# Kernel tuning notes

Hardware: AMD Instinct MI355X
Metric: run time of the kernel (lower is better)

## Reference

```python
import jax, jax.numpy as jnp
import numpy as np

N_NODES = 50000
N_EDGES = 800000
D_IN = 512
D_HID = 256


def gcn_conv(x, W, b, src, dst, n_nodes):
    """PyG-style GCNConv: self-loops + symmetric normalization.
    x: [N, d_in], W: [d_in, d_out], b: [d_out], src/dst: [E] (already include self-loops? no -> add here)
    """
    loops = jnp.arange(n_nodes, dtype=src.dtype)
    src_f = jnp.concatenate([src, loops])  # [E+N]
    dst_f = jnp.concatenate([dst, loops])
    deg = jax.ops.segment_sum(jnp.ones_like(dst_f, dtype=x.dtype), dst_f,
                              num_segments=n_nodes)  # [N]
    dinv = jnp.where(deg > 0, jax.lax.rsqrt(deg), 0.0)
    norm = dinv[src_f] * dinv[dst_f]  # [E+N]
    h = x @ W  # [N, d_out] -- dense GEMM
    msg = h[src_f] * norm[:, None]  # gather + scale, [E+N, d_out]
    out = jax.ops.segment_sum(msg, dst_f, num_segments=n_nodes)  # scatter-add
    return out + b


def setup_inputs() -> dict:
    key = jax.random.key(0)
    k1, k2, k3, k4, k5 = jax.random.split(key, 5)
    x = jax.random.normal(k1, (N_NODES, D_IN), dtype=jnp.float32)
    edge_index = jax.random.randint(k2, (2, N_EDGES), 0, N_NODES, dtype=jnp.int32)
    # Glorot-ish init for weights
    W1 = jax.random.normal(k3, (D_IN, D_HID), dtype=jnp.float32) / np.sqrt(D_IN)
    W2 = jax.random.normal(k4, (D_HID, D_HID), dtype=jnp.float32) / np.sqrt(D_HID)
    b1 = jnp.zeros((D_HID,), dtype=jnp.float32)
    b2 = jnp.zeros((D_HID,), dtype=jnp.float32)
    return {"x": x, "edge_index": edge_index, "W1": W1, "b1": b1, "W2": W2, "b2": b2}


def reference(x, edge_index, W1, b1, W2, b2):
    n_nodes = x.shape[0]
    src, dst = edge_index[0], edge_index[1]
    h = jax.nn.relu(gcn_conv(x, W1, b1, src, dst, n_nodes))
    h = gcn_conv(h, W2, b2, src, dst, n_nodes)
    # edge-level gather-dot scoring
    score = jnp.einsum('ed,ed->e', h[src], h[dst])  # [E]
    prob_edge = jax.nn.sigmoid(score)
    return prob_edge
```

## Files before the change

kernel.cpp:

```cpp
#include <hip/hip_runtime.h>
#include <stdint.h>

#define D_IN 512
#define D_HID 256

typedef __attribute__((ext_vector_type(8))) short bf16x8;
typedef __attribute__((ext_vector_type(8))) unsigned short u16x8;
typedef __attribute__((ext_vector_type(4))) float f32x4;

__device__ __forceinline__ float b2f(unsigned short u) {
    union { float f; uint32_t i; } x; x.i = ((uint32_t)u) << 16; return x.f;
}
__device__ __forceinline__ unsigned short f2b(float f) {
    union { float f; uint32_t i; } x; x.f = f;
    uint32_t i = x.i;
    uint32_t r = (i + 0x7FFFu + ((i >> 16) & 1u)) >> 16;
    return (unsigned short)r;
}

__device__ __forceinline__ void async_copy16(const unsigned short* g, unsigned short* lds) {
    __builtin_amdgcn_global_load_lds((const __attribute__((address_space(1))) unsigned int*)g,
                                     (__attribute__((address_space(3))) unsigned int*)lds,
                                     16, 0, 0);
}

__global__ __launch_bounds__(256) void detect_dtype_kernel(const ushort4* __restrict__ raw,
                                                           int n4, int* __restrict__ flag) {
    int i = blockIdx.x * blockDim.x + threadIdx.x;
    int hit = 0;
    if (i < n4) {
        ushort4 u = raw[i];
        hit = ((((u.x >> 7) & 0xFF) == 0xFF) || (((u.y >> 7) & 0xFF) == 0xFF) ||
               (((u.z >> 7) & 0xFF) == 0xFF) || (((u.w >> 7) & 0xFF) == 0xFF)) ? 1 : 0;
    }
    unsigned long long b = __ballot(hit);
    if ((threadIdx.x & 63) == 0 && b != 0ULL) atomicOr(flag, 1);
}

__global__ __launch_bounds__(256) void xcast_kernel(const void* __restrict__ X,
        unsigned short* __restrict__ xh, int n4, const int* __restrict__ flag) {
    int i = blockIdx.x * blockDim.x + threadIdx.x;
    if (i >= n4) return;
    ushort4 o;
    if (*flag != 0) {
        float4 v = ((const float4*)X)[i];
        o.x = f2b(v.x); o.y = f2b(v.y); o.z = f2b(v.z); o.w = f2b(v.w);
    } else {
        o = ((const ushort4*)X)[i];
    }
    ((ushort4*)xh)[i] = o;
}

__global__ void hist_kernel(const int* __restrict__ dst, int* __restrict__ counts, int E) {
    int e = blockIdx.x * blockDim.x + threadIdx.x;
    if (e < E) atomicAdd(&counts[dst[e]], 1);
}

__global__ __launch_bounds__(256) void partial_sum_kernel(const int* __restrict__ counts,
        int* __restrict__ partial, int n) {
    __shared__ int sh[4];
    int b = blockIdx.x;
    int lane = threadIdx.x & 63, wv = threadIdx.x >> 6;
    int s = 0;
    for (int j = threadIdx.x; j < 1024; j += 256) {
        int i = b * 1024 + j;
        s += (i < n) ? counts[i] : 0;
    }
#pragma unroll
    for (int off = 32; off > 0; off >>= 1) s += __shfl_down(s, off, 64);
    if (lane == 0) sh[wv] = s;
    __syncthreads();
    if (threadIdx.x == 0) partial[b] = sh[0] + sh[1] + sh[2] + sh[3];
}

__global__ void scan_partials_kernel(int* __restrict__ partial, int nb,
                                     int* __restrict__ indptr, int N) {
    int lane = threadIdx.x & 63;
    int orig = (lane < nb) ? partial[lane] : 0;
    int v = orig;
#pragma unroll
    for (int off = 1; off < 64; off <<= 1) {
        int u = __shfl(v, lane - off, 64);
        if (lane >= off) v += u;
    }
    int tot = __shfl(v, nb - 1, 64);
    if (lane < nb) partial[lane] = v - orig;
    if (lane == 0) indptr[N] = tot;
}

__global__ __launch_bounds__(1024) void scan_chunk_kernel(const int* __restrict__ counts,
        const int* __restrict__ partial, int* __restrict__ indptr, int* __restrict__ cursor,
        float* __restrict__ dinv, int n) {
    __shared__ int sh[1024];
    int b = blockIdx.x;
    int i = b * 1024 + threadIdx.x;
    int v = (i < n) ? counts[i] : 0;
    sh[threadIdx.x] = v;
    __syncthreads();
    for (int off = 1; off < 1024; off <<= 1) {
        int t = (threadIdx.x >= off) ? sh[threadIdx.x - off] : 0;
        __syncthreads();
        sh[threadIdx.x] += t;
        __syncthreads();
    }
    if (i < n) {
        int e = partial[b] + sh[threadIdx.x] - v;
        indptr[i] = e;
        cursor[i] = e;
        dinv[i] = rsqrtf((float)(v + 1));
    }
}

__global__ void scatter_kernel(const int* __restrict__ src, const int* __restrict__ dst,
                               int* __restrict__ cursor, int* __restrict__ csr_src,
                               int* __restrict__ csr_dst, int* __restrict__ csr_eid, int E) {
    int e = blockIdx.x * blockDim.x + threadIdx.x;
    if (e < E) {
        int d = dst[e];
        int pos = atomicAdd(&cursor[d], 1);
        csr_src[pos] = src[e];
        csr_dst[pos] = d;
        csr_eid[pos] = e;
    }
}

__global__ void wT_kernel(const void* __restrict__ W, unsigned short* __restrict__ WT,
                          int K, const int* __restrict__ flag) {
    int idx = blockIdx.x * blockDim.x + threadIdx.x;
    if (idx >= K * 256) return;
    int k = idx >> 8;
    int n = idx & 255;
    float v = (*flag != 0) ? ((const float*)W)[idx] : b2f(((const unsigned short*)W)[idx]);
    WT[n * K + k] = f2b(v);
}

template<int K>
__global__ __launch_bounds__(256) void gemm_bf16(const unsigned short* __restrict__ A,
        const unsigned short* __restrict__ WT, unsigned short* __restrict__ C, int M) {
    __shared__ unsigned short As[2][64 * 64];
    constexpr int NK = K / 64;
    int t = threadIdx.x;
    int lane = t & 63, wv = t >> 6;
    int n0 = lane & 15, grp = lane >> 4;
    int row0 = blockIdx.x * 64;

    int srow = wv * 16 + (lane >> 3);
    int segp = lane & 7;

    f32x4 acc[4][4];
#pragma unroll
    for (int rt = 0; rt < 4; ++rt)
#pragma unroll
        for (int ct = 0; ct < 4; ++ct) acc[rt][ct] = (f32x4){0.f, 0.f, 0.f, 0.f};

#pragma unroll
    for (int j = 0; j < 2; ++j) {
        int row = srow + j * 8;
        int s = (segp - row) & 7;
        const unsigned short* g = A + (size_t)min(row0 + row, M - 1) * K + s * 8;
        async_copy16(g, &As[0][0] + wv * 1024 + j * 512);
    }
    asm volatile("s_waitcnt vmcnt(0)" ::: "memory");
    __builtin_amdgcn_s_barrier();

    for (int kk = 0; kk < NK; ++kk) {
        int cur = kk & 1;
        if (kk + 1 < NK) {
            int kof = (kk + 1) * 64;
#pragma unroll
            for (int j = 0; j < 2; ++j) {
                int row = srow + j * 8;
                int s = (segp - row) & 7;
                const unsigned short* g = A + (size_t)min(row0 + row, M - 1) * K + kof + s * 8;
                async_copy16(g, &As[cur ^ 1][0] + wv * 1024 + j * 512);
            }
        }
        int kof = kk * 64;
        bf16x8 bw[4][2];
#pragma unroll
        for (int ct = 0; ct < 4; ++ct)
#pragma unroll
            for (int h = 0; h < 2; ++h)
                bw[ct][h] = *(const bf16x8*)(WT + (size_t)((wv * 4 + ct) * 16 + n0) * K
                                             + kof + h * 32 + grp * 8);
#pragma unroll
        for (int rt = 0; rt < 4; ++rt) {
            int r = rt * 16 + n0;
#pragma unroll
            for (int h = 0; h < 2; ++h) {
                int sp = (h * 4 + grp + r) & 7;
                bf16x8 a = *(const bf16x8*)(&As[cur][0] + r * 64 + sp * 8);
#pragma unroll
                for (int ct = 0; ct < 4; ++ct)
                    acc[rt][ct] = __builtin_amdgcn_mfma_f32_16x16x32_bf16(a, bw[ct][h],
                                                                          acc[rt][ct], 0, 0, 0);
            }
        }
        asm volatile("s_waitcnt vmcnt(0)" ::: "memory");
        __builtin_amdgcn_s_barrier();
    }
#pragma unroll
    for (int rt = 0; rt < 4; ++rt) {
#pragma unroll
        for (int ct = 0; ct < 4; ++ct) {
#pragma unroll
            for (int reg = 0; reg < 4; ++reg) {
                int row = row0 + rt * 16 + grp * 4 + reg;
                if (row < M)
                    C[(size_t)row * 256 + (wv * 4 + ct) * 16 + n0] = f2b(acc[rt][ct][reg]);
            }
        }
    }
}

__global__ __launch_bounds__(256) void aggregate_kernel(const unsigned short* __restrict__ h,
        const int* __restrict__ indptr, const int* __restrict__ csr_src,
        const float* __restrict__ dinv, const void* __restrict__ bias,
        unsigned short* __restrict__ out, int n, int do_relu, const int* __restrict__ flag) {
    int wave = threadIdx.x >> 6;
    int lane = threadIdx.x & 63;
    int half = lane >> 5;
    int hl = lane & 31;
    int v = blockIdx.x * 4 + wave;
    if (v >= n) return;
    int beg = indptr[v];
    int end = indptr[v + 1];
    float dv = dinv[v];

    float acc[8];
    if (half == 0) {
        u16x8 hv = *(const u16x8*)(h + (size_t)v * 256 + hl * 8);
#pragma unroll
        for (int i = 0; i < 8; ++i) acc[i] = dv * b2f(hv[i]);
    } else {
#pragma unroll
        for (int i = 0; i < 8; ++i) acc[i] = 0.f;
    }

    int eA = beg + half;
    float w0 = 0.f, w1 = 0.f, w2 = 0.f;
    u16x8 r0, r1, r2;
    if (eA < end) {
        int s = csr_src[eA];
        w0 = dinv[s];
        r0 = *(const u16x8*)(h + (size_t)s * 256 + hl * 8);
    }
    if (eA + 2 < end) {
        int s = csr_src[eA + 2];
        w1 = dinv[s];
        r1 = *(const u16x8*)(h + (size_t)s * 256 + hl * 8);
    }
    if (eA + 4 < end) {
        int s = csr_src[eA + 4];
        w2 = dinv[s];
        r2 = *(const u16x8*)(h + (size_t)s * 256 + hl * 8);
    }
    for (int e = eA; e < end; e += 2) {
#pragma unroll
        for (int i = 0; i < 8; ++i) acc[i] += w0 * b2f(r0[i]);
        w0 = w1; r0 = r1;
        w1 = w2; r1 = r2;
        int en = e + 6;
        if (en < end) {
            int s = csr_src[en];
            w2 = dinv[s];
            r2 = *(const u16x8*)(h + (size_t)s * 256 + hl * 8);
        }
    }

#pragma unroll
    for (int i = 0; i < 8; ++i) acc[i] += __shfl_xor(acc[i], 32, 64);

    if (half == 0) {
        float bb[8];
        if (*flag != 0) {
            const float* bp = (const float*)bias + hl * 8;
#pragma unroll
            for (int i = 0; i < 8; ++i) bb[i] = bp[i];
        } else {
            const unsigned short* bp = (const unsigned short*)bias + hl * 8;
#pragma unroll
            for (int i = 0; i < 8; ++i) bb[i] = b2f(bp[i]);
        }
        u16x8 ov;
#pragma unroll
        for (int i = 0; i < 8; ++i) {
            float o = dv * acc[i] + bb[i];
            if (do_relu) o = fmaxf(o, 0.f);
            ov[i] = f2b(o);
        }
        *(u16x8*)(out + (size_t)v * 256 + hl * 8) = ov;
    }
}

__global__ __launch_bounds__(256) void edge_score_mfma(const unsigned short* __restrict__ h,
        const int* __restrict__ csr_src, const int* __restrict__ csr_dst,
        const int* __restrict__ csr_eid,
        void* __restrict__ out, int E, const int* __restrict__ flag) {
    int lane = threadIdx.x & 63;
    int wv = threadIdx.x >> 6;
    int base = (blockIdx.x * 4 + wv) * 16;
    if (base >= E) return;
    int m = lane & 15, grp = lane >> 4;
    int e = base + m;
    int ec = min(e, E - 1);
    int s = csr_src[ec], d = csr_dst[ec];
    int eid = csr_eid[ec];
    const unsigned short* hs = h + (size_t)s * 256 + grp * 8;
    const unsigned short* hd = h + (size_t)d * 256 + grp * 8;
    f32x4 acc = {0.f, 0.f, 0.f, 0.f};
#pragma unroll
    for (int kk = 0; kk < 8; ++kk) {
        bf16x8 a = *(const bf16x8*)(hs + kk * 32);
        bf16x8 b = *(const bf16x8*)(hd + kk * 32);
        acc = __builtin_amdgcn_mfma_f32_16x16x32_bf16(a, b, acc, 0, 0, 0);
    }
    int reg = m - grp * 4;
    if (reg >= 0 && reg < 4 && e < E) {
        float p = (reg == 0) ? acc[0] : (reg == 1) ? acc[1] : (reg == 2) ? acc[2] : acc[3];
        float prob = 1.f / (1.f + __expf(-p));
        if (*flag != 0)
            ((float*)out)[eid] = prob;
        else
            ((unsigned short*)out)[eid] = f2b(prob);
    }
}

extern "C" void kernel_launch(void* const* d_in, const int* in_sizes, int n_in,
                              void* d_out, int out_size, void* d_ws, size_t ws_size,
                              hipStream_t stream) {
    const void* x  = d_in[0];
    const int* edge_index = (const int*)d_in[1];
    const void* W1 = d_in[2];
    const void* b1 = d_in[3];
    const void* W2 = d_in[4];
    const void* b2 = d_in[5];

    const int N = in_sizes[0] / D_IN;
    const int E = in_sizes[1] / 2;
    const int* src = edge_index;
    const int* dst = edge_index + E;

    char* ws = (char*)d_ws;
    size_t off = 0;
    auto alloc = [&](size_t bytes) {
        char* p = ws + off;
        off = (off + bytes + 255) & ~(size_t)255;
        return p;
    };
    int* flag     = (int*)alloc(256);
    float* dinv   = (float*)alloc((size_t)N * 4);
    int* counts   = (int*)alloc((size_t)N * 4);
    int* indptr   = (int*)alloc((size_t)(N + 1) * 4);
    int* cursor   = (int*)alloc((size_t)N * 4);
    int* partial  = (int*)alloc(64 * 4);
    int* csr_src  = (int*)alloc((size_t)E * 4);
    int* csr_dst  = (int*)alloc((size_t)E * 4);
    int* csr_eid  = (int*)alloc((size_t)E * 4);
    unsigned short* W1T = (unsigned short*)alloc((size_t)D_IN * 256 * 2);
    unsigned short* W2T = (unsigned short*)alloc((size_t)D_HID * 256 * 2);
    unsigned short* xh  = (unsigned short*)alloc((size_t)N * D_IN * 2);
    unsigned short* hA  = (unsigned short*)alloc((size_t)N * 256 * 2);
    unsigned short* hB  = (unsigned short*)alloc((size_t)N * 256 * 2);

    const int nb = (N + 1023) / 1024;

    hipMemsetAsync(flag, 0, 4, stream);
    hipMemsetAsync(counts, 0, (size_t)N * 4, stream);
    detect_dtype_kernel<<<64, 256, 0, stream>>>((const ushort4*)x, 16384, flag);
    xcast_kernel<<<(N * D_IN / 4 + 255) / 256, 256, 0, stream>>>(x, xh, N * D_IN / 4, flag);
    hist_kernel<<<(E + 255) / 256, 256, 0, stream>>>(dst, counts, E);
    partial_sum_kernel<<<nb, 256, 0, stream>>>(counts, partial, N);
    scan_partials_kernel<<<1, 64, 0, stream>>>(partial, nb, indptr, N);
    scan_chunk_kernel<<<nb, 1024, 0, stream>>>(counts, partial, indptr, cursor, dinv, N);
    scatter_kernel<<<(E + 255) / 256, 256, 0, stream>>>(src, dst, cursor, csr_src, csr_dst, csr_eid, E);
    wT_kernel<<<(D_IN * 256 + 255) / 256, 256, 0, stream>>>(W1, W1T, D_IN, flag);
    wT_kernel<<<(D_HID * 256 + 255) / 256, 256, 0, stream>>>(W2, W2T, D_HID, flag);

    int ggrid = (N + 63) / 64;
    gemm_bf16<D_IN><<<ggrid, 256, 0, stream>>>(xh, W1T, hA, N);
    aggregate_kernel<<<(N + 3) / 4, 256, 0, stream>>>(hA, indptr, csr_src, dinv, b1, hB, N, 1, flag);
    gemm_bf16<D_HID><<<ggrid, 256, 0, stream>>>(hB, W2T, hA, N);
    aggregate_kernel<<<(N + 3) / 4, 256, 0, stream>>>(hA, indptr, csr_src, dinv, b2, hB, N, 0, flag);
    edge_score_mfma<<<(E + 63) / 64, 256, 0, stream>>>(hB, csr_src, csr_dst, csr_eid, d_out, E, flag);
}
```

Measured before the change: 537.0 us.

## Fuse fp32-to-bf16 cast into first GEMM and coalesce edge output via permute

The separate xcast kernel, which wrote a bf16 copy of x, is removed. The first GEMM now loads fp32 x directly through registers, converts it, and stages it into LDS, which saves a full write and re-read of the converted input. Edge scores are now written contiguously in CSR order to a temp buffer and then permuted to original order by a gather kernel, replacing the scattered output writes. The cost is a synchronous register-staged load path instead of async LDS copies in the first GEMM, plus one extra small kernel and buffer.

```diff
diff --git a/kernel.cpp b/kernel.cpp
--- a/kernel.cpp
+++ b/kernel.cpp
@@ -35,20 +35,6 @@
     }
     unsigned long long b = __ballot(hit);
     if ((threadIdx.x & 63) == 0 && b != 0ULL) atomicOr(flag, 1);
-}
-
-__global__ __launch_bounds__(256) void xcast_kernel(const void* __restrict__ X,
-        unsigned short* __restrict__ xh, int n4, const int* __restrict__ flag) {
-    int i = blockIdx.x * blockDim.x + threadIdx.x;
-    if (i >= n4) return;
-    ushort4 o;
-    if (*flag != 0) {
-        float4 v = ((const float4*)X)[i];
-        o.x = f2b(v.x); o.y = f2b(v.y); o.z = f2b(v.z); o.w = f2b(v.w);
-    } else {
-        o = ((const ushort4*)X)[i];
-    }
-    ((ushort4*)xh)[i] = o;
 }
 
 __global__ void hist_kernel(const int* __restrict__ dst, int* __restrict__ counts, int E) {
@@ -113,14 +99,14 @@
 
 __global__ void scatter_kernel(const int* __restrict__ src, const int* __restrict__ dst,
                                int* __restrict__ cursor, int* __restrict__ csr_src,
-                               int* __restrict__ csr_dst, int* __restrict__ csr_eid, int E) {
+                               int* __restrict__ csr_dst, int* __restrict__ pos_of, int E) {
     int e = blockIdx.x * blockDim.x + threadIdx.x;
     if (e < E) {
         int d = dst[e];
         int pos = atomicAdd(&cursor[d], 1);
         csr_src[pos] = src[e];
         csr_dst[pos] = d;
-        csr_eid[pos] = e;
+        pos_of[e] = pos;
     }
 }
 
@@ -134,9 +120,10 @@
     WT[n * K + k] = f2b(v);
 }
 
-template<int K>
-__global__ __launch_bounds__(256) void gemm_bf16(const unsigned short* __restrict__ A,
-        const unsigned short* __restrict__ WT, unsigned short* __restrict__ C, int M) {
+template<int K, bool MF32>
+__global__ __launch_bounds__(256) void gemm_bf16(const void* __restrict__ Ain,
+        const unsigned short* __restrict__ WT, unsigned short* __restrict__ C, int M,
+        const int* __restrict__ flag) {
     __shared__ unsigned short As[2][64 * 64];
     constexpr int NK = K / 64;
     int t = threadIdx.x;
@@ -153,29 +140,7 @@
 #pragma unroll
         for (int ct = 0; ct < 4; ++ct) acc[rt][ct] = (f32x4){0.f, 0.f, 0.f, 0.f};
 
-#pragma unroll
-    for (int j = 0; j < 2; ++j) {
-        int row = srow + j * 8;
-        int s = (segp - row) & 7;
-        const unsigned short* g = A + (size_t)min(row0 + row, M - 1) * K + s * 8;
-        async_copy16(g, &As[0][0] + wv * 1024 + j * 512);
-    }
-    asm volatile("s_waitcnt vmcnt(0)" ::: "memory");
-    __builtin_amdgcn_s_barrier();
-
-    for (int kk = 0; kk < NK; ++kk) {
-        int cur = kk & 1;
-        if (kk + 1 < NK) {
-            int kof = (kk + 1) * 64;
-#pragma unroll
-            for (int j = 0; j < 2; ++j) {
-                int row = srow + j * 8;
-                int s = (segp - row) & 7;
-                const unsigned short* g = A + (size_t)min(row0 + row, M - 1) * K + kof + s * 8;
-                async_copy16(g, &As[cur ^ 1][0] + wv * 1024 + j * 512);
-            }
-        }
-        int kof = kk * 64;
+    auto compute_tile = [&](int kof, const unsigned short* Abuf) {
         bf16x8 bw[4][2];
 #pragma unroll
         for (int ct = 0; ct < 4; ++ct)
@@ -189,15 +154,78 @@
 #pragma unroll
             for (int h = 0; h < 2; ++h) {
                 int sp = (h * 4 + grp + r) & 7;
-                bf16x8 a = *(const bf16x8*)(&As[cur][0] + r * 64 + sp * 8);
+                bf16x8 a = *(const bf16x8*)(Abuf + r * 64 + sp * 8);
 #pragma unroll
                 for (int ct = 0; ct < 4; ++ct)
                     acc[rt][ct] = __builtin_amdgcn_mfma_f32_16x16x32_bf16(a, bw[ct][h],
                                                                           acc[rt][ct], 0, 0, 0);
             }
         }
+    };
+
+    bool f32src = MF32 && (*flag != 0);
+    if (f32src) {
+        const float* A = (const float*)Ain;
+        auto stage_f32 = [&](int kof, int buf, const float4* pr) {
+#pragma unroll
+            for (int j = 0; j < 2; ++j) {
+                u16x8 o;
+#pragma unroll
+                for (int q = 0; q < 4; ++q) {
+                    o[q]     = f2b(pr[j * 2 + 0][q]);
+                    o[q + 4] = f2b(pr[j * 2 + 1][q]);
+                }
+                *(u16x8*)(&As[buf][0] + wv * 1024 + j * 512 + lane * 8) = o;
+            }
+        };
+        auto load_f32 = [&](int kof, float4* pr) {
+#pragma unroll
+            for (int j = 0; j < 2; ++j) {
+                int row = srow + j * 8;
+                int s = (segp - row) & 7;
+                const float* g = A + (size_t)min(row0 + row, M - 1) * K + kof + s * 8;
+                pr[j * 2 + 0] = *(const float4*)(g);
+                pr[j * 2 + 1] = *(const float4*)(g + 4);
+            }
+        };
+        float4 pr[4];
+        load_f32(0, pr);
+        stage_f32(0, 0, pr);
+        for (int kk = 0; kk < NK; ++kk) {
+            int cur = kk & 1;
+            if (kk + 1 < NK) load_f32((kk + 1) * 64, pr);
+            asm volatile("s_waitcnt lgkmcnt(0)" ::: "memory");
+            __builtin_amdgcn_s_barrier();
+            compute_tile(kk * 64, &As[cur][0]);
+            if (kk + 1 < NK) stage_f32((kk + 1) * 64, cur ^ 1, pr);
+        }
+    } else {
+        const unsigned short* A = (const unsigned short*)Ain;
+#pragma unroll
+        for (int j = 0; j < 2; ++j) {
+            int row = srow + j * 8;
+            int s = (segp - row) & 7;
+            const unsigned short* g = A + (size_t)min(row0 + row, M - 1) * K + s * 8;
+            async_copy16(g, &As[0][0] + wv * 1024 + j * 512);
+        }
         asm volatile("s_waitcnt vmcnt(0)" ::: "memory");
         __builtin_amdgcn_s_barrier();
+        for (int kk = 0; kk < NK; ++kk) {
+            int cur = kk & 1;
+            if (kk + 1 < NK) {
+                int kof = (kk + 1) * 64;
+#pragma unroll
+                for (int j = 0; j < 2; ++j) {
+                    int row = srow + j * 8;
+                    int s = (segp - row) & 7;
+                    const unsigned short* g = A + (size_t)min(row0 + row, M - 1) * K + kof + s * 8;
+                    async_copy16(g, &As[cur ^ 1][0] + wv * 1024 + j * 512);
+                }
+            }
+            compute_tile(kk * 64, &As[cur][0]);
+            asm volatile("s_waitcnt vmcnt(0)" ::: "memory");
+            __builtin_amdgcn_s_barrier();
+        }
     }
 #pragma unroll
     for (int rt = 0; rt < 4; ++rt) {
@@ -295,8 +323,7 @@
 
 __global__ __launch_bounds__(256) void edge_score_mfma(const unsigned short* __restrict__ h,
         const int* __restrict__ csr_src, const int* __restrict__ csr_dst,
-        const int* __restrict__ csr_eid,
-        void* __restrict__ out, int E, const int* __restrict__ flag) {
+        float* __restrict__ tmp, int E) {
     int lane = threadIdx.x & 63;
     int wv = threadIdx.x >> 6;
     int base = (blockIdx.x * 4 + wv) * 16;
@@ -305,7 +332,6 @@
     int e = base + m;
     int ec = min(e, E - 1);
     int s = csr_src[ec], d = csr_dst[ec];
-    int eid = csr_eid[ec];
     const unsigned short* hs = h + (size_t)s * 256 + grp * 8;
     const unsigned short* hd = h + (size_t)d * 256 + grp * 8;
     f32x4 acc = {0.f, 0.f, 0.f, 0.f};
@@ -318,12 +344,20 @@
     int reg = m - grp * 4;
     if (reg >= 0 && reg < 4 && e < E) {
         float p = (reg == 0) ? acc[0] : (reg == 1) ? acc[1] : (reg == 2) ? acc[2] : acc[3];
-        float prob = 1.f / (1.f + __expf(-p));
-        if (*flag != 0)
-            ((float*)out)[eid] = prob;
-        else
-            ((unsigned short*)out)[eid] = f2b(prob);
-    }
+        tmp[e] = 1.f / (1.f + __expf(-p));
+    }
+}
+
+__global__ __launch_bounds__(256) void permute_out_kernel(const float* __restrict__ tmp,
+        const int* __restrict__ pos_of, void* __restrict__ out, int E,
+        const int* __restrict__ flag) {
+    int e = blockIdx.x * blockDim.x + threadIdx.x;
+    if (e >= E) return;
+    float p = tmp[pos_of[e]];
+    if (*flag != 0)
+        ((float*)out)[e] = p;
+    else
+        ((unsigned short*)out)[e] = f2b(p);
 }
 
 extern "C" void kernel_launch(void* const* d_in, const int* in_sizes, int n_in,
@@ -356,10 +390,10 @@
     int* partial  = (int*)alloc(64 * 4);
     int* csr_src  = (int*)alloc((size_t)E * 4);
     int* csr_dst  = (int*)alloc((size_t)E * 4);
-    int* csr_eid  = (int*)alloc((size_t)E * 4);
+    int* pos_of   = (int*)alloc((size_t)E * 4);
+    float* ptmp   = (float*)alloc((size_t)E * 4);
     unsigned short* W1T = (unsigned short*)alloc((size_t)D_IN * 256 * 2);
     unsigned short* W2T = (unsigned short*)alloc((size_t)D_HID * 256 * 2);
-    unsigned short* xh  = (unsigned short*)alloc((size_t)N * D_IN * 2);
     unsigned short* hA  = (unsigned short*)alloc((size_t)N * 256 * 2);
     unsigned short* hB  = (unsigned short*)alloc((size_t)N * 256 * 2);
 
@@ -368,19 +402,19 @@
     hipMemsetAsync(flag, 0, 4, stream);
     hipMemsetAsync(counts, 0, (size_t)N * 4, stream);
     detect_dtype_kernel<<<64, 256, 0, stream>>>((const ushort4*)x, 16384, flag);
-    xcast_kernel<<<(N * D_IN / 4 + 255) / 256, 256, 0, stream>>>(x, xh, N * D_IN / 4, flag);
     hist_kernel<<<(E + 255) / 256, 256, 0, stream>>>(dst, counts, E);
     partial_sum_kernel<<<nb, 256, 0, stream>>>(counts, partial, N);
     scan_partials_kernel<<<1, 64, 0, stream>>>(partial, nb, indptr, N);
     scan_chunk_kernel<<<nb, 1024, 0, stream>>>(counts, partial, indptr, cursor, dinv, N);
-    scatter_kernel<<<(E + 255) / 256, 256, 0, stream>>>(src, dst, cursor, csr_src, csr_dst, csr_eid, E);
+    scatter_kernel<<<(E + 255) / 256, 256, 0, stream>>>(src, dst, cursor, csr_src, csr_dst, pos_of, E);
     wT_kernel<<<(D_IN * 256 + 255) / 256, 256, 0, stream>>>(W1, W1T, D_IN, flag);
     wT_kernel<<<(D_HID * 256 + 255) / 256, 256, 0, stream>>>(W2, W2T, D_HID, flag);
 
     int ggrid = (N + 63) / 64;
-    gemm_bf16<D_IN><<<ggrid, 256, 0, stream>>>(xh, W1T, hA, N);
+    gemm_bf16<D_IN, true><<<ggrid, 256, 0, stream>>>(x, W1T, hA, N, flag);
     aggregate_kernel<<<(N + 3) / 4, 256, 0, stream>>>(hA, indptr, csr_src, dinv, b1, hB, N, 1, flag);
-    gemm_bf16<D_HID><<<ggrid, 256, 0, stream>>>(hB, W2T, hA, N);
+    gemm_bf16<D_HID, false><<<ggrid, 256, 0, stream>>>(hB, W2T, hA, N, flag);
     aggregate_kernel<<<(N + 3) / 4, 256, 0, stream>>>(hA, indptr, csr_src, dinv, b2, hB, N, 0, flag);
-    edge_score_mfma<<<(E + 63) / 64, 256, 0, stream>>>(hB, csr_src, csr_dst, csr_eid, d_out, E, flag);
-}
+    edge_score_mfma<<<(E + 63) / 64, 256, 0, stream>>>(hB, csr_src, csr_dst, ptmp, E);
+    permute_out_kernel<<<(E + 255) / 256, 256, 0, stream>>>(ptmp, pos_of, d_out, E, flag);
+}
```

Result: faster. 516.4 us (-3.8%).
